# Kernel optimization log

Hardware: AMD Instinct MI355X
Metric: run time of the kernel (lower is better)

## Reference

```python
import jax, jax.numpy as jnp
import numpy as np

PI = float(np.pi)
BN_EPS = 1e-3
LN_EPS = 1e-5


def ssslu(x, shape, bias):
    # x * (sin(softsign(x) * shape*pi/2) + (bias + 1))
    s = x / (1.0 + jnp.abs(x))
    return x * (jnp.sin(s * (shape * PI / 2.0)) + (bias + 1.0))


def bn(x, g, b, m, v):
    inv = (g / jnp.sqrt(v + BN_EPS))[None, :, None, None]
    return (x - m[None, :, None, None]) * inv + b[None, :, None, None]


def conv2d(x, w, bias=None, pad=0):
    y = jax.lax.conv_general_dilated(x, w, (1, 1), [(pad, pad), (pad, pad)],
                                     dimension_numbers=('NCHW', 'OIHW', 'NCHW'))
    if bias is not None:
        y = y + bias[None, :, None, None]
    return y


def ln_silu(v):
    # LayerNorm (unit weight, zero bias) over last axis, then SiLU
    mu = jnp.mean(v, axis=-1, keepdims=True)
    var = jnp.mean(jnp.square(v - mu), axis=-1, keepdims=True)
    h = (v - mu) / jnp.sqrt(var + LN_EPS)
    return h * jax.nn.sigmoid(h)


def _forward(x, w_qkv, g_qkv, b_qkv, m_qkv, v_qkv,
             w_co, g_co, b_co, m_co, v_co,
             w_b1, bias_b1, g_b1, b_b1, m_b1, v_b1,
             w_b2, bias_b2, g_b2, b_b2, m_b2, v_b2):
    B, C, H, W = x.shape
    Q = (w_qkv.shape[0] - C) // 2
    # qkv Conv block: conv1x1 -> SSSLU(-3, 0.3) -> BN
    t = bn(ssslu(conv2d(x, w_qkv, pad=0), -3.0, 0.3), g_qkv, b_qkv, m_qkv, v_qkv)
    xq, xk, xv = jnp.split(t, [Q, 2 * Q], axis=1)
    # max-pooled Q/K rows and columns -> [B*Q, W] / [B*Q, H]
    qw = jnp.max(xq, axis=2).reshape(B * Q, W)
    kw = jnp.max(xk, axis=2).reshape(B * Q, W)
    qh = jnp.max(xq, axis=3).reshape(B * Q, H)
    kh = jnp.max(xk, axis=3).reshape(B * Q, H)
    # xaw[i,b] = max_a qw[i,a]*kw[i,b]; xah[i,a] = max_b qh[i,a]*kh[i,b]
    xaw = jnp.max(qw[:, :, None] * kw[:, None, :], axis=1)  # [BQ, W]
    xah = jnp.max(qh[:, :, None] * kh[:, None, :], axis=2)  # [BQ, H]
    xaw = ln_silu(xaw)
    xah = ln_silu(xah)
    xa = (xah[:, :, None] * xaw[:, None, :]).reshape(B, Q, H, W)
    # co: SSSLUConv(Q+C -> Q): conv3x3 -> BN -> SSSLU(1.0, 0)
    xa = jnp.concatenate([xa, xv], axis=1)
    xa = ssslu(bn(conv2d(xa, w_co, pad=1), g_co, b_co, m_co, v_co), 1.0, 0.0)
    # back[0]: Conv(Q -> C, k3, bias): conv -> SSSLU(-3, 0.3) -> BN
    xa = bn(ssslu(conv2d(xa, w_b1, bias_b1, pad=1), -3.0, 0.3), g_b1, b_b1, m_b1, v_b1)
    # back[1]: SSSLUConv(C -> C, k1, bias): conv -> BN -> SSSLU(0.8, 0)
    xa = ssslu(bn(conv2d(xa, w_b2, bias_b2, pad=0), g_b2, b_b2, m_b2, v_b2), 0.8, 0.0)
    # back[2]: Sigmoid; source returns the gate itself
    return jax.nn.sigmoid(xa)


def setup_inputs() -> dict:
    B, C, Q, H, W = 16, 256, 256, 64, 64
    key = jax.random.key(0)
    ks = jax.random.split(key, 32)

    def w_init(k, o, i, kh, kw):
        return jax.random.normal(k, (o, i, kh, kw), jnp.float32) * (1.0 / np.sqrt(i * kh * kw))

    def bn_params(k, c):
        k1, k2, k3, k4 = jax.random.split(k, 4)
        g = jax.random.uniform(k1, (c,), jnp.float32, 0.5, 1.5)
        b = jax.random.normal(k2, (c,), jnp.float32) * 0.1
        m = jax.random.normal(k3, (c,), jnp.float32) * 0.1
        v = jax.random.uniform(k4, (c,), jnp.float32, 0.5, 1.5)
        return g, b, m, v

    x = jax.random.normal(ks[0], (B, C, H, W), jnp.float32)
    w_qkv = w_init(ks[1], 2 * Q + C, C, 1, 1)
    g_qkv, b_qkv, m_qkv, v_qkv = bn_params(ks[2], 2 * Q + C)
    w_co = w_init(ks[3], Q, Q + C, 3, 3)
    g_co, b_co, m_co, v_co = bn_params(ks[4], Q)
    w_b1 = w_init(ks[5], C, Q, 3, 3)
    bias_b1 = jax.random.normal(ks[6], (C,), jnp.float32) * 0.05
    g_b1, b_b1, m_b1, v_b1 = bn_params(ks[7], C)
    w_b2 = w_init(ks[8], C, C, 1, 1)
    bias_b2 = jax.random.normal(ks[9], (C,), jnp.float32) * 0.05
    g_b2, b_b2, m_b2, v_b2 = bn_params(ks[10], C)
    return dict(x=x, w_qkv=w_qkv, g_qkv=g_qkv, b_qkv=b_qkv, m_qkv=m_qkv, v_qkv=v_qkv,
                w_co=w_co, g_co=g_co, b_co=b_co, m_co=m_co, v_co=v_co,
                w_b1=w_b1, bias_b1=bias_b1, g_b1=g_b1, b_b1=b_b1, m_b1=m_b1, v_b1=v_b1,
                w_b2=w_b2, bias_b2=bias_b2, g_b2=g_b2, b_b2=b_b2, m_b2=m_b2, v_b2=v_b2)


def reference(x, w_qkv, g_qkv, b_qkv, m_qkv, v_qkv,
              w_co, g_co, b_co, m_co, v_co,
              w_b1, bias_b1, g_b1, b_b1, m_b1, v_b1,
              w_b2, bias_b2, g_b2, b_b2, m_b2, v_b2):
    return _forward(x, w_qkv, g_qkv, b_qkv, m_qkv, v_qkv,
                    w_co, g_co, b_co, m_co, v_co,
                    w_b1, bias_b1, g_b1, b_b1, m_b1, v_b1,
                    w_b2, bias_b2, g_b2, b_b2, m_b2, v_b2)
```

## Files before the change

kernel.cpp:

```cpp
#include <hip/hip_runtime.h>
#include <hip/hip_bf16.h>
#include <math.h>

#define PI_F 3.14159265358979323846f

typedef unsigned short u16;
typedef unsigned int   u32;
typedef float    f32x4 __attribute__((ext_vector_type(4)));
typedef _Float16 f16x8 __attribute__((ext_vector_type(8)));
typedef u16      u16x8 __attribute__((ext_vector_type(8)));
typedef u16      u16x4 __attribute__((ext_vector_type(4)));

__device__ __forceinline__ u16 f2h(float f){ union{ _Float16 h; u16 u; } c; c.h = (_Float16)f; return c.u; }
__device__ __forceinline__ float h2f(u16 u){ union{ u16 u; _Float16 h; } c; c.u = u; return (float)c.h; }

__device__ __forceinline__ void gl16(const void* g, void* l){
  __builtin_amdgcn_global_load_lds((const __attribute__((address_space(1))) u32*)g,
                                   (__attribute__((address_space(3))) u32*)l, 16, 0, 0);
}

__device__ __forceinline__ int SWZ(int r){ return (r>>1)&3; }

__device__ __forceinline__ float wred_max(float v){
#pragma unroll
  for (int m = 32; m; m >>= 1) v = fmaxf(v, __shfl_xor(v, m));
  return v;
}
__device__ __forceinline__ float wred_min(float v){
#pragma unroll
  for (int m = 32; m; m >>= 1) v = fminf(v, __shfl_xor(v, m));
  return v;
}
__device__ __forceinline__ float wred_sum(float v){
#pragma unroll
  for (int m = 32; m; m >>= 1) v += __shfl_xor(v, m);
  return v;
}

__device__ __forceinline__ float ssslu_f(float x, float shp, float bp1){
  float s = x / (1.0f + fabsf(x));
  return x * (__sinf(s * shp) + bp1);
}

__device__ __forceinline__ float epi_val(float v, float4 p, float shp, float bp1, int ORDER, bool SIG){
  v += p.w;
  if (ORDER == 0){ v = ssslu_f(v, shp, bp1); v = (v - p.z) * p.x + p.y; }
  else           { v = (v - p.z) * p.x + p.y; v = ssslu_f(v, shp, bp1); }
  if (SIG) v = 1.f / (1.f + __expf(-v));
  return v;
}

__device__ __forceinline__ void atomicMaxF(float* a, float v){
  if (v >= 0.f) atomicMax(reinterpret_cast<int*>(a), __float_as_int(v));
  else          atomicMin(reinterpret_cast<unsigned int*>(a), __float_as_uint(v));
}

__device__ __forceinline__ f16x8 mul8h(u16x8 a, u16x8 b){
  union{ u16x8 u; f16x8 h; } A, B; A.u = a; B.u = b;
  return A.h * B.h;
}

__global__ __launch_bounds__(256)
void xpose_k(const float* __restrict__ X, u16* __restrict__ XH)
{
  __shared__ u16 L[16384];
  const int tid = threadIdx.x;
  const int b = blockIdx.x >> 6, h = blockIdx.x & 63;
  const float* xp = X + (size_t)b * 256 * 4096 + h * 64;
#pragma unroll
  for (int i = 0; i < 16; ++i){
    int ci = i * 16 + (tid >> 4);
    int w4 = (tid & 15) * 4;
    float4 v = *(const float4*)(xp + (size_t)ci * 4096 + w4);
    int sw = 4 * ((ci >> 3) & 15);
    u16x4 d;
    d[0] = f2h(v.x); d[1] = f2h(v.y); d[2] = f2h(v.z); d[3] = f2h(v.w);
    *(u16x4*)&L[ci * 64 + (w4 ^ sw)] = d;
  }
  __syncthreads();
  u16* out = XH + (((size_t)b * 4096 + (size_t)h * 64) << 8);
#pragma unroll
  for (int it = 0; it < 8; ++it){
    int w   = it * 8 + (tid >> 5);
    int m   = tid & 31;
    int ci0 = m * 8;
    int base = (w & ~3) ^ (4 * (m & 15));
    int wl   = w & 3;
    u16x8 o;
#pragma unroll
    for (int k = 0; k < 8; ++k)
      o[k] = L[(ci0 + k) * 64 + base + wl];
    *(u16x8*)&out[w * 256 + ci0] = o;
  }
}

template<int CI_T, bool CAT>
__global__ __launch_bounds__(256, 2)
void conv3_mfma(const u16* __restrict__ Apk, const u16* __restrict__ Bg,
                u16* __restrict__ DstH, const float4* __restrict__ pp,
                const u16* __restrict__ xahT_, const u16* __restrict__ xawT_,
                float shp, float bp1, int ORDER)
{
  constexpr int NCC = CI_T / 32;
  constexpr int NIT = NCC * 3;
  __shared__ __align__(16) u16 sAB[36864];

  const int tid  = threadIdx.x;
  const int lane = tid & 63;
  const int wv   = tid >> 6;
  const int wn   = wv;
  const int l15  = lane & 15, l4 = lane >> 4;

  const int bx  = blockIdx.x;
  const int bid = (bx & 7) * 32 + (bx >> 3);
  const int b   = bid >> 4;
  const int r0  = (bid & 15) * 4;
  const int m0  = blockIdx.y * 128;

  auto STAGE_A = [&](int it2){
    int d2 = it2 % 3, c2 = it2 / 3;
    int bufA = it2 & 1;
#pragma unroll
    for (int j2 = 0; j2 < 3; ++j2){
      int tap = d2 * 3 + j2;
      const u16* base = Apk + (size_t)tap * 256 * CI_T + (size_t)m0 * CI_T + c2 * 32;
#pragma unroll
      for (int i = 0; i < 2; ++i){
        int row = i * 64 + (tid >> 2);
        int s   = tid & 3;
        const u16* src = base + (size_t)row * CI_T + ((s ^ SWZ(row)) << 3);
        gl16(src, &sAB[bufA * 12288 + j2 * 4096 + (i * 64 + wv * 16) * 32]);
      }
    }
  };
  auto STAGE_B = [&](int c2){
#pragma unroll
    for (int j = 0; j < 6; ++j){
      int rr  = j;
      int hh  = r0 - 1 + rr; hh = min(63, max(0, hh));
      int w   = tid >> 2, s = tid & 3;
      int ci0 = c2 * 32 + ((s ^ SWZ(w + 1)) << 3);
      if (CAT && c2 < 8){
        u16x8 vh = *(const u16x8*)&xahT_[((b * 64 + hh) << 8) + ci0];
        u16x8 vw = *(const u16x8*)&xawT_[((b * 64 + w ) << 8) + ci0];
        *(f16x8*)&sAB[24576 + rr * 2048 + w * 32 + s * 8] = mul8h(vh, vw);
      } else {
        int ci = CAT ? (ci0 - 256) : ci0;
        const u16* src = Bg + (((size_t)b * 4096 + hh * 64 + w) << 8) + ci;
        gl16(src, &sAB[24576 + rr * 2048 + wv * 512]);
      }
    }
  };

  f32x4 acc[8][4];
#pragma unroll
  for (int i = 0; i < 8; ++i)
#pragma unroll
    for (int j = 0; j < 4; ++j){ acc[i][j][0]=0.f; acc[i][j][1]=0.f; acc[i][j][2]=0.f; acc[i][j][3]=0.f; }

  STAGE_A(0);

  for (int it = 0; it < NIT; ++it){
    const int d = it % 3, c = it / 3;
    const int bufA = it & 1;

    if (it + 1 < NIT) STAGE_A(it + 1);
    if (d == 0){
      STAGE_B(c);
      __syncthreads();
    }

    const int brow = wn + d;
    const bool rowok = ((unsigned)(r0 + wn + d - 1)) < 64u;

#pragma unroll
    for (int dw = 0; dw < 3; ++dw){
      f16x8 afr[8], bfr[4];
#pragma unroll
      for (int fm = 0; fm < 8; ++fm){
        int m  = fm * 16 + l15;
        int sl = l4 ^ SWZ(m);
        afr[fm] = *(const f16x8*)&sAB[bufA * 12288 + dw * 4096 + m * 32 + sl * 8];
      }
#pragma unroll
      for (int fn = 0; fn < 4; ++fn){
        int w_in = fn * 16 + l15 + dw - 1;
        int wc   = min(63, max(0, w_in));
        int sl2  = l4 ^ SWZ(wc + 1);
        f16x8 t  = *(const f16x8*)&sAB[24576 + brow * 2048 + wc * 32 + sl2 * 8];
        bool ok  = rowok && (((unsigned)w_in) < 64u);
        bfr[fn]  = ok ? t : (f16x8)(_Float16)0;
      }
      __builtin_amdgcn_s_setprio(1);
#pragma unroll
      for (int fm = 0; fm < 8; ++fm)
#pragma unroll
        for (int fn = 0; fn < 4; ++fn)
          acc[fm][fn] = __builtin_amdgcn_mfma_f32_16x16x32_f16(afr[fm], bfr[fn], acc[fm][fn], 0, 0, 0);
      __builtin_amdgcn_s_setprio(0);
    }
    __syncthreads();
  }

  const int h = r0 + wn;
#pragma unroll
  for (int fm = 0; fm < 8; ++fm){
    const int cobase = m0 + fm * 16 + 4 * l4;
    float4 P0 = pp[cobase], P1 = pp[cobase+1], P2 = pp[cobase+2], P3 = pp[cobase+3];
#pragma unroll
    for (int fn = 0; fn < 4; ++fn){
      int w = fn * 16 + l15;
      float v0 = epi_val(acc[fm][fn][0], P0, shp, bp1, ORDER, false);
      float v1 = epi_val(acc[fm][fn][1], P1, shp, bp1, ORDER, false);
      float v2 = epi_val(acc[fm][fn][2], P2, shp, bp1, ORDER, false);
      float v3 = epi_val(acc[fm][fn][3], P3, shp, bp1, ORDER, false);
      uint2 st;
      st.x = (u32)f2h(v0) | ((u32)f2h(v1) << 16);
      st.y = (u32)f2h(v2) | ((u32)f2h(v3) << 16);
      *(uint2*)&DstH[(((size_t)b * 4096 + (size_t)h * 64 + w) << 8) + cobase] = st;
    }
  }
}

template<int EPI>
__global__ __launch_bounds__(512, 2)
void conv1_big(const u16* __restrict__ Apk, const u16* __restrict__ Bg,
               u16* __restrict__ DstH, float* __restrict__ DstF,
               const float4* __restrict__ pp,
               float shp, float bp1, int ORDER)
{
  __shared__ __align__(16) u16 sA[2][8192];
  __shared__ __align__(16) u16 sB[2][8192];

  const int tid  = threadIdx.x;
  const int lane = tid & 63;
  const int wv   = tid >> 6;
  const int wm   = wv >> 2;
  const int wn   = wv & 3;
  const int l15  = lane & 15, l4 = lane >> 4;

  const int bx  = blockIdx.x;
  const int bid = (bx & 7) * 32 + (bx >> 3);
  const int b   = bid >> 4;
  const int h0  = (bid & 15) * 4;

  auto STAGE = [&](int c){
    int buf = c & 1;
#pragma unroll
    for (int j = 0; j < 2; ++j){
      int g = j * 512 + tid;
      int m = g >> 2, s = g & 3;
      const u16* srcA = Apk + (size_t)m * 256 + c * 32 + ((s ^ SWZ(m)) << 3);
      gl16(srcA, &sA[buf][(j * 512 + wv * 64) * 8]);
      int r = g >> 8, w = (g >> 2) & 63;
      const u16* srcB = Bg + (((size_t)b * 4096 + (h0 + r) * 64 + w) << 8) + c * 32 + ((s ^ SWZ(w)) << 3);
      gl16(srcB, &sB[buf][(j * 512 + wv * 64) * 8]);
    }
  };

  f32x4 acc[8][4];
#pragma unroll
  for (int i = 0; i < 8; ++i)
#pragma unroll
    for (int j = 0; j < 4; ++j){ acc[i][j][0]=0.f; acc[i][j][1]=0.f; acc[i][j][2]=0.f; acc[i][j][3]=0.f; }

  STAGE(0);
  __syncthreads();

  for (int c = 0; c < 8; ++c){
    if (c + 1 < 8) STAGE(c + 1);
    const int buf = c & 1;
    f16x8 afr[8], bfr[4];
#pragma unroll
    for (int fm = 0; fm < 8; ++fm){
      int m  = wm * 128 + fm * 16 + l15;
      int sl = l4 ^ SWZ(m);
      afr[fm] = *(const f16x8*)&sA[buf][m * 32 + sl * 8];
    }
#pragma unroll
    for (int fn = 0; fn < 4; ++fn){
      int w  = fn * 16 + l15;
      int sl = l4 ^ SWZ(w);
      bfr[fn] = *(const f16x8*)&sB[buf][(wn * 64 + w) * 32 + sl * 8];
    }
    __builtin_amdgcn_s_setprio(1);
#pragma unroll
    for (int fm = 0; fm < 8; ++fm)
#pragma unroll
      for (int fn = 0; fn < 4; ++fn)
        acc[fm][fn] = __builtin_amdgcn_mfma_f32_16x16x32_f16(afr[fm], bfr[fn], acc[fm][fn], 0, 0, 0);
    __builtin_amdgcn_s_setprio(0);
    __syncthreads();
  }

  const int h = h0 + wn;
#pragma unroll
  for (int fm = 0; fm < 8; ++fm){
    const int cobase = wm * 128 + fm * 16 + 4 * l4;
    float4 P0 = pp[cobase], P1 = pp[cobase+1], P2 = pp[cobase+2], P3 = pp[cobase+3];
#pragma unroll
    for (int fn = 0; fn < 4; ++fn){
      int w = fn * 16 + l15;
      if (EPI == 1){
        float v0 = epi_val(acc[fm][fn][0], P0, shp, bp1, ORDER, false);
        float v1 = epi_val(acc[fm][fn][1], P1, shp, bp1, ORDER, false);
        float v2 = epi_val(acc[fm][fn][2], P2, shp, bp1, ORDER, false);
        float v3 = epi_val(acc[fm][fn][3], P3, shp, bp1, ORDER, false);
        uint2 st;
        st.x = (u32)f2h(v0) | ((u32)f2h(v1) << 16);
        st.y = (u32)f2h(v2) | ((u32)f2h(v3) << 16);
        *(uint2*)&DstH[(((size_t)b * 4096 + (size_t)h * 64 + w) << 8) + cobase] = st;
      } else {
        float v0 = epi_val(acc[fm][fn][0], P0, shp, bp1, ORDER, true);
        float v1 = epi_val(acc[fm][fn][1], P1, shp, bp1, ORDER, true);
        float v2 = epi_val(acc[fm][fn][2], P2, shp, bp1, ORDER, true);
        float v3 = epi_val(acc[fm][fn][3], P3, shp, bp1, ORDER, true);
        size_t base = ((size_t)(b * 256 + cobase)) * 4096 + (size_t)h * 64 + w;
        DstF[base]          = v0;
        DstF[base + 4096]   = v1;
        DstF[base + 2*4096] = v2;
        DstF[base + 3*4096] = v3;
      }
    }
  }
}

template<int SRC, int EPI, int HLOOP>
__global__ __launch_bounds__(256)
void conv_mfma(const u16* __restrict__ Apk, const u16* __restrict__ Bg,
               u16* __restrict__ DstH, float* __restrict__ DstF,
               const float4* __restrict__ pp,
               const float* __restrict__ Xf,
               float* __restrict__ qwp, float* __restrict__ kwp,
               float* __restrict__ qhp, float* __restrict__ khp,
               float shp, float bp1, int ORDER, int M)
{
  constexpr int NCC = 8;
  constexpr int HG  = 64 / HLOOP;
  __shared__ __align__(16) u16 sA[2][8192];
  __shared__ __align__(16) u16 sB[2][2112];

  const int tid  = threadIdx.x;
  const int lane = tid & 63;
  const int wv   = tid >> 6;
  const int bx   = blockIdx.x;
  const int b    = bx / HG;
  const int h0   = (bx % HG) * HLOOP;
  const int m0   = blockIdx.y * 256;

  f32x4 acc[4][4];
  f32x4 cmax[4][4];
  if (EPI == 0){
#pragma unroll
    for (int i = 0; i < 4; ++i)
#pragma unroll
      for (int j = 0; j < 4; ++j){ cmax[i][j][0]=-3.0e38f; cmax[i][j][1]=-3.0e38f; cmax[i][j][2]=-3.0e38f; cmax[i][j][3]=-3.0e38f; }
  }

  for (int hi = 0; hi < HLOOP; ++hi){
    const int h = h0 + hi;
#pragma unroll
    for (int i = 0; i < 4; ++i)
#pragma unroll
      for (int j = 0; j < 4; ++j){ acc[i][j][0]=0.f; acc[i][j][1]=0.f; acc[i][j][2]=0.f; acc[i][j][3]=0.f; }

    auto stageA = [&](int c, int buf){
      const u16* base = Apk + (size_t)m0 * 256 + c * 32;
#pragma unroll
      for (int i = 0; i < 4; ++i){
        int row = i * 64 + (tid >> 2);
        int s   = tid & 3;
        const u16* src = base + (size_t)row * 256 + ((s ^ SWZ(row)) << 3);
        gl16(src, &sA[buf][(i * 64 + wv * 16) * 32]);
      }
    };
    auto stageB = [&](int c, int buf){
      const int w = tid >> 2, s = tid & 3, r = w + 1;
      const u16* src = Bg + (((size_t)b * 4096 + h * 64 + w) << 8) + c * 32 + ((s ^ SWZ(r)) << 3);
      gl16(src, &sB[buf][(1 + wv * 16) * 32]);
    };

    __syncthreads();
    stageA(0, 0);
    stageB(0, 0);
    __syncthreads();

    for (int it = 0; it < NCC; ++it){
      if (it + 1 < NCC){ stageA(it + 1, (it + 1) & 1); stageB(it + 1, (it + 1) & 1); }
      f16x8 afr[4], bfr[4];
#pragma unroll
      for (int fm = 0; fm < 4; ++fm){
        int row = wv * 64 + fm * 16 + (lane & 15);
        int sl  = (lane >> 4) ^ SWZ(row);
        afr[fm] = *(const f16x8*)&sA[it & 1][row * 32 + sl * 8];
      }
#pragma unroll
      for (int fn = 0; fn < 4; ++fn){
        int r  = fn * 16 + (lane & 15) + 1;
        int sl = (lane >> 4) ^ SWZ(r);
        bfr[fn] = *(const f16x8*)&sB[it & 1][r * 32 + sl * 8];
      }
      __builtin_amdgcn_s_setprio(1);
#pragma unroll
      for (int fm = 0; fm < 4; ++fm)
#pragma unroll
        for (int fn = 0; fn < 4; ++fn)
          acc[fm][fn] = __builtin_amdgcn_mfma_f32_16x16x32_f16(afr[fm], bfr[fn], acc[fm][fn], 0, 0, 0);
      __builtin_amdgcn_s_setprio(0);
      __syncthreads();
    }

    const int l15 = lane & 15, l4 = lane >> 4;
    if (EPI == 0){
#pragma unroll
      for (int fm = 0; fm < 4; ++fm){
        const int cobase = m0 + wv * 64 + fm * 16 + 4 * l4;
        float4 P0 = pp[cobase], P1 = pp[cobase+1], P2 = pp[cobase+2], P3 = pp[cobase+3];
        f32x4 ev[4];
#pragma unroll
        for (int fn = 0; fn < 4; ++fn){
          ev[fn][0] = epi_val(acc[fm][fn][0], P0, shp, bp1, ORDER, false);
          ev[fn][1] = epi_val(acc[fm][fn][1], P1, shp, bp1, ORDER, false);
          ev[fn][2] = epi_val(acc[fm][fn][2], P2, shp, bp1, ORDER, false);
          ev[fn][3] = epi_val(acc[fm][fn][3], P3, shp, bp1, ORDER, false);
#pragma unroll
          for (int r = 0; r < 4; ++r) cmax[fm][fn][r] = fmaxf(cmax[fm][fn][r], ev[fn][r]);
        }
#pragma unroll
        for (int r = 0; r < 4; ++r){
          float mv = fmaxf(fmaxf(ev[0][r], ev[1][r]), fmaxf(ev[2][r], ev[3][r]));
          mv = fmaxf(mv, __shfl_xor(mv, 1));
          mv = fmaxf(mv, __shfl_xor(mv, 2));
          mv = fmaxf(mv, __shfl_xor(mv, 4));
          mv = fmaxf(mv, __shfl_xor(mv, 8));
          if (l15 == 0){
            int q = (cobase + r) & 255;
            float* rowp = (m0 == 0) ? qhp : khp;
            rowp[(((b << 8) | q) << 6) + h] = mv;
          }
        }
      }
    }
  }

  if (EPI == 0){
    const int l15 = lane & 15, l4 = lane >> 4;
    float* colp = (m0 == 0) ? qwp : kwp;
#pragma unroll
    for (int fm = 0; fm < 4; ++fm)
#pragma unroll
      for (int fn = 0; fn < 4; ++fn)
#pragma unroll
        for (int r = 0; r < 4; ++r){
          int q = (m0 + wv * 64 + fm * 16 + 4 * l4 + r) & 255;
          int w = fn * 16 + l15;
          atomicMaxF(&colp[(((b << 8) | q) << 6) + w], cmax[fm][fn][r]);
        }
  }
}

__device__ __forceinline__ float ln_silu_wave(float v){
  float mu = wred_sum(v) * (1.f / 64.f);
  float d = v - mu;
  float var = wred_sum(d * d) * (1.f / 64.f);
  float hn = d * rsqrtf(var + 1e-5f);
  return hn / (1.f + __expf(-hn));
}

__global__ void attn_k(const float* __restrict__ qw, const float* __restrict__ kw,
                       const float* __restrict__ qh, const float* __restrict__ kh,
                       u16* __restrict__ xahT, u16* __restrict__ xawT)
{
  int row  = blockIdx.x * 4 + (threadIdx.x >> 6);
  int lane = threadIdx.x & 63;
  int idx  = (row << 6) + lane;
  float qwv = qw[idx], kwv = kw[idx], qhv = qh[idx], khv = kh[idx];
  float Pq = wred_max(qwv), mq = wred_min(qwv);
  float Pk = wred_max(khv), mk = wred_min(khv);
  float aw = fmaxf(kwv * Pq, kwv * mq);
  float ah = fmaxf(qhv * Pk, qhv * mk);
  aw = ln_silu_wave(aw);
  ah = ln_silu_wave(ah);
  int b = row >> 8, q = row & 255;
  xawT[((b * 64 + lane) << 8) + q] = f2h(aw);
  xahT[((b * 64 + lane) << 8) + q] = f2h(ah);
}

__global__ void pack_k(const float* __restrict__ wqkv, const float* __restrict__ wco,
                       const float* __restrict__ wb1, const float* __restrict__ wb2,
                       const float* gq, const float* bq, const float* mq, const float* vq,
                       const float* gc, const float* bc, const float* mc, const float* vc,
                       const float* g1, const float* b1, const float* m1, const float* v1, const float* bias1,
                       const float* g2, const float* b2, const float* m2, const float* v2, const float* bias2,
                       u16* __restrict__ WQ, u16* __restrict__ WCO, u16* __restrict__ WB1, u16* __restrict__ WB2,
                       float4* __restrict__ PP)
{
  const int E0 = 196608, E1 = 196608 + 1179648, E2 = 196608 + 1179648 + 589824, E3 = 2031616;
  int i = blockIdx.x * 256 + threadIdx.x;
  if (i >= E3 + 1536) return;
  if (i < E0){ WQ[i] = f2h(wqkv[i]); }
  else if (i < E1){
    int d = i - E0; int tap = d / 131072; int rm = d % 131072; int m = rm >> 9; int ci = rm & 511;
    WCO[d] = f2h(wco[(size_t)((m << 9) | ci) * 9 + tap]);
  } else if (i < E2){
    int d = i - E1; int tap = d / 65536; int rm = d & 65535; int m = rm >> 8; int ci = rm & 255;
    WB1[d] = f2h(wb1[(size_t)((m << 8) | ci) * 9 + tap]);
  } else if (i < E3){
    int d = i - E2; WB2[d] = f2h(wb2[d]);
  } else {
    int c = i - E3;
    float g, be, mm, vv, bi;
    if (c < 768){ g = gq[c]; be = bq[c]; mm = mq[c]; vv = vq[c]; bi = 0.f; }
    else if (c < 1024){ int j = c - 768;  g = gc[j]; be = bc[j]; mm = mc[j]; vv = vc[j]; bi = 0.f; }
    else if (c < 1280){ int j = c - 1024; g = g1[j]; be = b1[j]; mm = m1[j]; vv = v1[j]; bi = bias1[j]; }
    else              { int j = c - 1280; g = g2[j]; be = b2[j]; mm = m2[j]; vv = v2[j]; bi = bias2[j]; }
    PP[c] = make_float4(g / sqrtf(vv + 1e-3f), be, mm, bi);
  }
}

__global__ void initpool_k(float* __restrict__ p)
{
  int i = blockIdx.x * 1024 + threadIdx.x * 4;
  float4 v = make_float4(-3.0e38f, -3.0e38f, -3.0e38f, -3.0e38f);
  *(float4*)(p + i) = v;
}

extern "C" void kernel_launch(void* const* d_in, const int* in_sizes, int n_in,
                              void* d_out, int out_size, void* d_ws, size_t ws_size,
                              hipStream_t stream)
{
  const float* x       = (const float*)d_in[0];
  const float* w_qkv   = (const float*)d_in[1];
  const float* g_qkv   = (const float*)d_in[2];
  const float* b_qkv   = (const float*)d_in[3];
  const float* m_qkv   = (const float*)d_in[4];
  const float* v_qkv   = (const float*)d_in[5];
  const float* w_co    = (const float*)d_in[6];
  const float* g_co    = (const float*)d_in[7];
  const float* b_co    = (const float*)d_in[8];
  const float* m_co    = (const float*)d_in[9];
  const float* v_co    = (const float*)d_in[10];
  const float* w_b1    = (const float*)d_in[11];
  const float* bias_b1 = (const float*)d_in[12];
  const float* g_b1    = (const float*)d_in[13];
  const float* b_b1    = (const float*)d_in[14];
  const float* m_b1    = (const float*)d_in[15];
  const float* v_b1    = (const float*)d_in[16];
  const float* w_b2    = (const float*)d_in[17];
  const float* bias_b2 = (const float*)d_in[18];
  const float* g_b2    = (const float*)d_in[19];
  const float* b_b2    = (const float*)d_in[20];
  const float* m_b2    = (const float*)d_in[21];
  const float* v_b2    = (const float*)d_in[22];
  float* out = (float*)d_out;

  char* W = (char*)d_ws;
  u16*    WQ   = (u16*)(W + 0);
  u16*    WCO  = (u16*)(W + 393216);
  u16*    WB1  = (u16*)(W + 2752512);
  u16*    WB2  = (u16*)(W + 3932160);
  float4* PP   = (float4*)(W + 4063232);
  u16*    TV   = (u16*)(W + 4087808);
  u16*    XAHT = (u16*)(W + 37642240);
  u16*    XAWT = (u16*)(W + 38166528);
  u16*    XH   = (u16*)(W + 38690816);
  u16*    Y1   = (u16*)(W + 38690816);
  u16*    Y2   = TV;
  float*  qw_  = (float*)(W + 72245248);
  float*  kw_  = (float*)(W + 73293824);
  float*  qh_  = (float*)(W + 74342400);
  float*  kh_  = (float*)(W + 75390976);

  const size_t NEED = 76439552;
  if (ws_size < NEED) return;

  const float SHP_N3 = -3.0f * PI_F * 0.5f;
  const float SHP_1  =  1.0f * PI_F * 0.5f;
  const float SHP_08 =  0.8f * PI_F * 0.5f;

  dim3 blk(256);

  pack_k<<<7942, blk, 0, stream>>>(w_qkv, w_co, w_b1, w_b2,
      g_qkv, b_qkv, m_qkv, v_qkv,
      g_co,  b_co,  m_co,  v_co,
      g_b1,  b_b1,  m_b1,  v_b1,  bias_b1,
      g_b2,  b_b2,  m_b2,  v_b2,  bias_b2,
      WQ, WCO, WB1, WB2, PP);

  initpool_k<<<512, blk, 0, stream>>>(qw_);

  xpose_k<<<1024, blk, 0, stream>>>(x, XH);

  conv_mfma<1, 0, 4><<<dim3(256, 2), blk, 0, stream>>>(
      WQ, XH, nullptr, nullptr, PP, nullptr,
      qw_, kw_, qh_, kh_, SHP_N3, 1.3f, 0, 512);

  conv1_big<1><<<256, 512, 0, stream>>>(
      WQ + (size_t)512 * 256, XH, TV, nullptr, PP + 512, SHP_N3, 1.3f, 0);

  attn_k<<<1024, blk, 0, stream>>>(qw_, kw_, qh_, kh_, XAHT, XAWT);

  conv3_mfma<512, true><<<dim3(256, 2), blk, 0, stream>>>(
      WCO, TV, Y1, PP + 768, XAHT, XAWT, SHP_1, 1.0f, 1);

  conv3_mfma<256, false><<<dim3(256, 2), blk, 0, stream>>>(
      WB1, Y1, Y2, PP + 1024, nullptr, nullptr, SHP_N3, 1.3f, 0);

  conv1_big<2><<<256, 512, 0, stream>>>(
      WB2, Y2, nullptr, out, PP + 1280, SHP_08, 1.0f, 1);
}
```

Baseline: 455.4 us.

## Replace atomic column max-pool with per-block partial pools reduced in attention kernel

The Q/K 1x1 conv kernel is rewritten with 512-thread blocks that each compute 4 rows of h at once (256x256 tile). Column max-pooling is done through shared memory, and per-block partials are written to workspace instead of using global float atomics. The attention kernel then reduces the 16 partials per row, which removes the init-pool launch and the atomic contention. The costs are extra partial-buffer traffic, which aliases the TV region and forces attn_k to run before conv1_big, and higher register pressure from the 8x4 accumulator tile.

```diff
diff --git a/kernel.cpp b/kernel.cpp
--- a/kernel.cpp
+++ b/kernel.cpp
@@ -48,11 +48,6 @@
   else           { v = (v - p.z) * p.x + p.y; v = ssslu_f(v, shp, bp1); }
   if (SIG) v = 1.f / (1.f + __expf(-v));
   return v;
-}
-
-__device__ __forceinline__ void atomicMaxF(float* a, float v){
-  if (v >= 0.f) atomicMax(reinterpret_cast<int*>(a), __float_as_int(v));
-  else          atomicMin(reinterpret_cast<unsigned int*>(a), __float_as_uint(v));
 }
 
 __device__ __forceinline__ f16x8 mul8h(u16x8 a, u16x8 b){
@@ -325,106 +320,101 @@
   }
 }
 
-template<int SRC, int EPI, int HLOOP>
-__global__ __launch_bounds__(256)
-void conv_mfma(const u16* __restrict__ Apk, const u16* __restrict__ Bg,
-               u16* __restrict__ DstH, float* __restrict__ DstF,
-               const float4* __restrict__ pp,
-               const float* __restrict__ Xf,
-               float* __restrict__ qwp, float* __restrict__ kwp,
-               float* __restrict__ qhp, float* __restrict__ khp,
-               float shp, float bp1, int ORDER, int M)
-{
-  constexpr int NCC = 8;
-  constexpr int HG  = 64 / HLOOP;
-  __shared__ __align__(16) u16 sA[2][8192];
-  __shared__ __align__(16) u16 sB[2][2112];
+__global__ __launch_bounds__(512, 2)
+void conv1_pool(const u16* __restrict__ Apk0, const u16* __restrict__ Bg,
+                const float4* __restrict__ pp0,
+                float* __restrict__ qhp, float* __restrict__ khp,
+                float* __restrict__ qwp, float* __restrict__ kwp,
+                float shp, float bp1)
+{
+  __shared__ __align__(16) u16 S[32768];
+  u16*   sA   = S;
+  u16*   sB   = S + 16384;
+  float* pool = (float*)S;
 
   const int tid  = threadIdx.x;
   const int lane = tid & 63;
   const int wv   = tid >> 6;
+  const int wm   = wv >> 2;
+  const int wn   = wv & 3;
+  const int l15  = lane & 15, l4 = lane >> 4;
+
   const int bx   = blockIdx.x;
-  const int b    = bx / HG;
-  const int h0   = (bx % HG) * HLOOP;
+  const int bid  = (bx & 7) * 32 + (bx >> 3);
+  const int b    = bid >> 4;
+  const int hblk = bid & 15;
+  const int h0   = hblk * 4;
   const int m0   = blockIdx.y * 256;
 
-  f32x4 acc[4][4];
-  f32x4 cmax[4][4];
-  if (EPI == 0){
-#pragma unroll
-    for (int i = 0; i < 4; ++i)
-#pragma unroll
-      for (int j = 0; j < 4; ++j){ cmax[i][j][0]=-3.0e38f; cmax[i][j][1]=-3.0e38f; cmax[i][j][2]=-3.0e38f; cmax[i][j][3]=-3.0e38f; }
-  }
-
-  for (int hi = 0; hi < HLOOP; ++hi){
-    const int h = h0 + hi;
-#pragma unroll
-    for (int i = 0; i < 4; ++i)
-#pragma unroll
-      for (int j = 0; j < 4; ++j){ acc[i][j][0]=0.f; acc[i][j][1]=0.f; acc[i][j][2]=0.f; acc[i][j][3]=0.f; }
-
-    auto stageA = [&](int c, int buf){
-      const u16* base = Apk + (size_t)m0 * 256 + c * 32;
-#pragma unroll
-      for (int i = 0; i < 4; ++i){
-        int row = i * 64 + (tid >> 2);
-        int s   = tid & 3;
-        const u16* src = base + (size_t)row * 256 + ((s ^ SWZ(row)) << 3);
-        gl16(src, &sA[buf][(i * 64 + wv * 16) * 32]);
-      }
-    };
-    auto stageB = [&](int c, int buf){
-      const int w = tid >> 2, s = tid & 3, r = w + 1;
-      const u16* src = Bg + (((size_t)b * 4096 + h * 64 + w) << 8) + c * 32 + ((s ^ SWZ(r)) << 3);
-      gl16(src, &sB[buf][(1 + wv * 16) * 32]);
-    };
-
+  const u16*    Apk = Apk0 + (size_t)m0 * 256;
+  const float4* pp  = pp0 + m0;
+  float* rowp = (blockIdx.y == 0) ? qhp : khp;
+  float* colp = (blockIdx.y == 0) ? qwp : kwp;
+
+  auto STAGE = [&](int c){
+    int buf = c & 1;
+#pragma unroll
+    for (int j = 0; j < 2; ++j){
+      int g = j * 512 + tid;
+      int m = g >> 2, s = g & 3;
+      const u16* srcA = Apk + (size_t)m * 256 + c * 32 + ((s ^ SWZ(m)) << 3);
+      gl16(srcA, &sA[buf * 8192 + (j * 512 + wv * 64) * 8]);
+      int r = g >> 8, w = (g >> 2) & 63;
+      const u16* srcB = Bg + (((size_t)b * 4096 + (h0 + r) * 64 + w) << 8) + c * 32 + ((s ^ SWZ(w)) << 3);
+      gl16(srcB, &sB[buf * 8192 + (j * 512 + wv * 64) * 8]);
+    }
+  };
+
+  f32x4 acc[8][4];
+#pragma unroll
+  for (int i = 0; i < 8; ++i)
+#pragma unroll
+    for (int j = 0; j < 4; ++j){ acc[i][j][0]=0.f; acc[i][j][1]=0.f; acc[i][j][2]=0.f; acc[i][j][3]=0.f; }
+
+  STAGE(0);
+  __syncthreads();
+
+  for (int c = 0; c < 8; ++c){
+    if (c + 1 < 8) STAGE(c + 1);
+    const int buf = c & 1;
+    f16x8 afr[8], bfr[4];
+#pragma unroll
+    for (int fm = 0; fm < 8; ++fm){
+      int m  = wm * 128 + fm * 16 + l15;
+      int sl = l4 ^ SWZ(m);
+      afr[fm] = *(const f16x8*)&sA[buf * 8192 + m * 32 + sl * 8];
+    }
+#pragma unroll
+    for (int fn = 0; fn < 4; ++fn){
+      int w  = fn * 16 + l15;
+      int sl = l4 ^ SWZ(w);
+      bfr[fn] = *(const f16x8*)&sB[buf * 8192 + (wn * 64 + w) * 32 + sl * 8];
+    }
+    __builtin_amdgcn_s_setprio(1);
+#pragma unroll
+    for (int fm = 0; fm < 8; ++fm)
+#pragma unroll
+      for (int fn = 0; fn < 4; ++fn)
+        acc[fm][fn] = __builtin_amdgcn_mfma_f32_16x16x32_f16(afr[fm], bfr[fn], acc[fm][fn], 0, 0, 0);
+    __builtin_amdgcn_s_setprio(0);
     __syncthreads();
-    stageA(0, 0);
-    stageB(0, 0);
-    __syncthreads();
-
-    for (int it = 0; it < NCC; ++it){
-      if (it + 1 < NCC){ stageA(it + 1, (it + 1) & 1); stageB(it + 1, (it + 1) & 1); }
-      f16x8 afr[4], bfr[4];
-#pragma unroll
-      for (int fm = 0; fm < 4; ++fm){
-        int row = wv * 64 + fm * 16 + (lane & 15);
-        int sl  = (lane >> 4) ^ SWZ(row);
-        afr[fm] = *(const f16x8*)&sA[it & 1][row * 32 + sl * 8];
-      }
-#pragma unroll
-      for (int fn = 0; fn < 4; ++fn){
-        int r  = fn * 16 + (lane & 15) + 1;
-        int sl = (lane >> 4) ^ SWZ(r);
-        bfr[fn] = *(const f16x8*)&sB[it & 1][r * 32 + sl * 8];
-      }
-      __builtin_amdgcn_s_setprio(1);
-#pragma unroll
-      for (int fm = 0; fm < 4; ++fm)
-#pragma unroll
-        for (int fn = 0; fn < 4; ++fn)
-          acc[fm][fn] = __builtin_amdgcn_mfma_f32_16x16x32_f16(afr[fm], bfr[fn], acc[fm][fn], 0, 0, 0);
-      __builtin_amdgcn_s_setprio(0);
-      __syncthreads();
-    }
-
-    const int l15 = lane & 15, l4 = lane >> 4;
-    if (EPI == 0){
-#pragma unroll
-      for (int fm = 0; fm < 4; ++fm){
-        const int cobase = m0 + wv * 64 + fm * 16 + 4 * l4;
-        float4 P0 = pp[cobase], P1 = pp[cobase+1], P2 = pp[cobase+2], P3 = pp[cobase+3];
-        f32x4 ev[4];
+  }
+
+  const int h = h0 + wn;
+#pragma unroll
+  for (int k = 0; k < 4; ++k){
+    if (wn == k){
+#pragma unroll
+      for (int fm = 0; fm < 8; ++fm){
+        const int cl = wm * 128 + fm * 16 + 4 * l4;
+        float4 P0 = pp[cl], P1 = pp[cl+1], P2 = pp[cl+2], P3 = pp[cl+3];
+        float ev[4][4];
 #pragma unroll
         for (int fn = 0; fn < 4; ++fn){
-          ev[fn][0] = epi_val(acc[fm][fn][0], P0, shp, bp1, ORDER, false);
-          ev[fn][1] = epi_val(acc[fm][fn][1], P1, shp, bp1, ORDER, false);
-          ev[fn][2] = epi_val(acc[fm][fn][2], P2, shp, bp1, ORDER, false);
-          ev[fn][3] = epi_val(acc[fm][fn][3], P3, shp, bp1, ORDER, false);
-#pragma unroll
-          for (int r = 0; r < 4; ++r) cmax[fm][fn][r] = fmaxf(cmax[fm][fn][r], ev[fn][r]);
+          ev[fn][0] = epi_val(acc[fm][fn][0], P0, shp, bp1, 0, false);
+          ev[fn][1] = epi_val(acc[fm][fn][1], P1, shp, bp1, 0, false);
+          ev[fn][2] = epi_val(acc[fm][fn][2], P2, shp, bp1, 0, false);
+          ev[fn][3] = epi_val(acc[fm][fn][3], P3, shp, bp1, 0, false);
         }
 #pragma unroll
         for (int r = 0; r < 4; ++r){
@@ -433,29 +423,25 @@
           mv = fmaxf(mv, __shfl_xor(mv, 2));
           mv = fmaxf(mv, __shfl_xor(mv, 4));
           mv = fmaxf(mv, __shfl_xor(mv, 8));
-          if (l15 == 0){
-            int q = (cobase + r) & 255;
-            float* rowp = (m0 == 0) ? qhp : khp;
-            rowp[(((b << 8) | q) << 6) + h] = mv;
+          if (l15 == 0)
+            rowp[(((b << 8) | (cl + r)) << 6) + h] = mv;
+        }
+#pragma unroll
+        for (int fn = 0; fn < 4; ++fn)
+#pragma unroll
+          for (int r = 0; r < 4; ++r){
+            int idx = ((cl + r) << 6) + fn * 16 + l15;
+            pool[idx] = (k == 0) ? ev[fn][r] : fmaxf(pool[idx], ev[fn][r]);
           }
-        }
       }
     }
-  }
-
-  if (EPI == 0){
-    const int l15 = lane & 15, l4 = lane >> 4;
-    float* colp = (m0 == 0) ? qwp : kwp;
-#pragma unroll
-    for (int fm = 0; fm < 4; ++fm)
-#pragma unroll
-      for (int fn = 0; fn < 4; ++fn)
-#pragma unroll
-        for (int r = 0; r < 4; ++r){
-          int q = (m0 + wv * 64 + fm * 16 + 4 * l4 + r) & 255;
-          int w = fn * 16 + l15;
-          atomicMaxF(&colp[(((b << 8) | q) << 6) + w], cmax[fm][fn][r]);
-        }
+    __syncthreads();
+  }
+  float* cbase = colp + (((size_t)(b * 16 + hblk)) << 14);
+#pragma unroll
+  for (int j = 0; j < 8; ++j){
+    int fi = j * 512 + tid;
+    *(float4*)&cbase[fi * 4] = *(const float4*)&pool[fi * 4];
   }
 }
 
@@ -467,21 +453,28 @@
   return hn / (1.f + __expf(-hn));
 }
 
-__global__ void attn_k(const float* __restrict__ qw, const float* __restrict__ kw,
+__global__ void attn_k(const float* __restrict__ qwp, const float* __restrict__ kwp,
                        const float* __restrict__ qh, const float* __restrict__ kh,
                        u16* __restrict__ xahT, u16* __restrict__ xawT)
 {
   int row  = blockIdx.x * 4 + (threadIdx.x >> 6);
   int lane = threadIdx.x & 63;
   int idx  = (row << 6) + lane;
-  float qwv = qw[idx], kwv = kw[idx], qhv = qh[idx], khv = kh[idx];
+  int b = row >> 8, q = row & 255;
+  size_t pb = ((size_t)b << 18) + (q << 6) + lane;
+  float qwv = -3.0e38f, kwv = -3.0e38f;
+#pragma unroll
+  for (int hb = 0; hb < 16; ++hb){
+    qwv = fmaxf(qwv, qwp[pb + ((size_t)hb << 14)]);
+    kwv = fmaxf(kwv, kwp[pb + ((size_t)hb << 14)]);
+  }
+  float qhv = qh[idx], khv = kh[idx];
   float Pq = wred_max(qwv), mq = wred_min(qwv);
   float Pk = wred_max(khv), mk = wred_min(khv);
   float aw = fmaxf(kwv * Pq, kwv * mq);
   float ah = fmaxf(qhv * Pk, qhv * mk);
   aw = ln_silu_wave(aw);
   ah = ln_silu_wave(ah);
-  int b = row >> 8, q = row & 255;
   xawT[((b * 64 + lane) << 8) + q] = f2h(aw);
   xahT[((b * 64 + lane) << 8) + q] = f2h(ah);
 }
@@ -516,13 +509,6 @@
     else              { int j = c - 1280; g = g2[j]; be = b2[j]; mm = m2[j]; vv = v2[j]; bi = bias2[j]; }
     PP[c] = make_float4(g / sqrtf(vv + 1e-3f), be, mm, bi);
   }
-}
-
-__global__ void initpool_k(float* __restrict__ p)
-{
-  int i = blockIdx.x * 1024 + threadIdx.x * 4;
-  float4 v = make_float4(-3.0e38f, -3.0e38f, -3.0e38f, -3.0e38f);
-  *(float4*)(p + i) = v;
 }
 
 extern "C" void kernel_launch(void* const* d_in, const int* in_sizes, int n_in,
@@ -560,18 +546,18 @@
   u16*    WB1  = (u16*)(W + 2752512);
   u16*    WB2  = (u16*)(W + 3932160);
   float4* PP   = (float4*)(W + 4063232);
+  float*  qwp_ = (float*)(W + 4087808);
+  float*  kwp_ = (float*)(W + 20865024);
   u16*    TV   = (u16*)(W + 4087808);
   u16*    XAHT = (u16*)(W + 37642240);
   u16*    XAWT = (u16*)(W + 38166528);
   u16*    XH   = (u16*)(W + 38690816);
   u16*    Y1   = (u16*)(W + 38690816);
   u16*    Y2   = TV;
-  float*  qw_  = (float*)(W + 72245248);
-  float*  kw_  = (float*)(W + 73293824);
-  float*  qh_  = (float*)(W + 74342400);
-  float*  kh_  = (float*)(W + 75390976);
-
-  const size_t NEED = 76439552;
+  float*  qh_  = (float*)(W + 72245248);
+  float*  kh_  = (float*)(W + 73293824);
+
+  const size_t NEED = 74342400;
   if (ws_size < NEED) return;
 
   const float SHP_N3 = -3.0f * PI_F * 0.5f;
@@ -587,19 +573,16 @@
       g_b2,  b_b2,  m_b2,  v_b2,  bias_b2,
       WQ, WCO, WB1, WB2, PP);
 
-  initpool_k<<<512, blk, 0, stream>>>(qw_);
-
   xpose_k<<<1024, blk, 0, stream>>>(x, XH);
 
-  conv_mfma<1, 0, 4><<<dim3(256, 2), blk, 0, stream>>>(
-      WQ, XH, nullptr, nullptr, PP, nullptr,
-      qw_, kw_, qh_, kh_, SHP_N3, 1.3f, 0, 512);
+  conv1_pool<<<dim3(256, 2), 512, 0, stream>>>(
+      WQ, XH, PP, qh_, kh_, qwp_, kwp_, SHP_N3, 1.3f);
+
+  attn_k<<<1024, blk, 0, stream>>>(qwp_, kwp_, qh_, kh_, XAHT, XAWT);
 
   conv1_big<1><<<256, 512, 0, stream>>>(
       WQ + (size_t)512 * 256, XH, TV, nullptr, PP + 512, SHP_N3, 1.3f, 0);
 
-  attn_k<<<1024, blk, 0, stream>>>(qw_, kw_, qh_, kh_, XAHT, XAWT);
-
   conv3_mfma<512, true><<<dim3(256, 2), blk, 0, stream>>>(
       WCO, TV, Y1, PP + 768, XAHT, XAWT, SHP_1, 1.0f, 1);
 
```

After: 450.0 us. No clear change (-1.2%).
